# Optimization experiments

Measured on AMD Instinct MI355X. Metric: run time of the kernel, lower is better.

Reference implementation:

```python
import jax, jax.numpy as jnp
import numpy as np

NFILTS = 6  # module-level global in the original repo


def setup_inputs() -> dict:
    key = jax.random.key(0)
    k = jax.random.split(key, 6)
    N, T, D, E = 128, 256, 10, NFILTS
    merged = jax.random.normal(k[0], (N, T, 14), dtype=jnp.float32)
    y_pred_i = jax.random.normal(k[1], (N, T, E), dtype=jnp.float32)
    y_pred_ij = jax.random.normal(k[2], (N, N, T, E), dtype=jnp.float32)
    # input1 holds flux errors in channels [1+nfilts : -2]; keep them bounded away from 0
    input1 = jax.random.uniform(k[3], (N, T, 1 + E + E + 2), dtype=jnp.float32) + 0.5
    samples = jax.random.normal(k[4], (N, D), dtype=jnp.float32)
    labels = jax.random.randint(k[5], (N,), 0, 10, dtype=jnp.int64)
    return {"merged": merged, "y_pred_i": y_pred_i, "y_pred_ij": y_pred_ij,
            "input1": input1, "samples": samples, "labels": labels}


def reference(merged, y_pred_i, y_pred_ij, input1, samples, labels):
    # err_true: [N, T, E]
    err_true = input1[:, :, 1 + NFILTS:-2]
    # pairwise latent distance: S_ij[i,j] = mean_d (samples[j] - samples[i])^2 -> [N, N]
    d = samples[None, :, :] - samples[:, None, :]
    S_ij = jnp.mean(d * d, axis=-1)
    # second term: mean over (T, E) of (y_pred_ij[i,j] - y_pred_i[j])^2 / err_true[j]^2 / 10
    diffsq = jnp.square(y_pred_ij - y_pred_i[None, :, :, :])          # [N, N, T, E]
    second = jnp.mean(diffsq / jnp.square(err_true)[None], axis=(2, 3)) / 10.0  # [N, N]
    avg_term = 0.5 * (second + second.T)
    L_sim = jnp.mean(jnp.abs(S_ij - avg_term))
    return L_sim
```

## Files before the change

### kernel.cpp

```cpp
#include <hip/hip_runtime.h>
#include <hip/hip_bf16.h>

#define NN 128
#define TT 256
#define EE 6
#define DD 10
#define TE (TT*EE)
#define C1 15

__global__ void prep_w(const float* __restrict__ input1, float* __restrict__ w) {
    int idx = blockIdx.x * 256 + threadIdx.x;
    if (idx < NN * TE) {
        int f = idx % TE;
        int j = idx / TE;
        int t = f / EE, e = f % EE;
        float v = input1[(j * TT + t) * C1 + 1 + EE + e];
        w[idx] = 1.0f / (v * v);
    }
}

__launch_bounds__(128)
__global__ void pair_reduce(const float* __restrict__ yij,
                            const float* __restrict__ yi,
                            const float* __restrict__ w,
                            float* __restrict__ raw) {
    const int j = blockIdx.x;
    const int i = blockIdx.y;
    const int tid = threadIdx.x;

    const float4* a  = (const float4*)(yij + ((size_t)i * NN + j) * TE);
    const float4* m  = (const float4*)(yi  + (size_t)j * TE);
    const float4* wv = (const float4*)(w   + (size_t)j * TE);

    float s = 0.0f;
#pragma unroll
    for (int k = 0; k < 3; ++k) {
        int f = tid + k * 128;
        float4 x  = a[f];
        float4 mm = m[f];
        float4 ww = wv[f];
        float d0 = x.x - mm.x; s += d0 * d0 * ww.x;
        float d1 = x.y - mm.y; s += d1 * d1 * ww.y;
        float d2 = x.z - mm.z; s += d2 * d2 * ww.z;
        float d3 = x.w - mm.w; s += d3 * d3 * ww.w;
    }
#pragma unroll
    for (int off = 32; off > 0; off >>= 1) s += __shfl_down(s, off);

    __shared__ float ls[2];
    if ((tid & 63) == 0) ls[tid >> 6] = s;
    __syncthreads();
    if (tid == 0) raw[i * NN + j] = ls[0] + ls[1];
}

__launch_bounds__(256)
__global__ void finalize(const float* __restrict__ raw,
                         const float* __restrict__ samples,
                         float* __restrict__ out) {
    __shared__ float smp[NN * DD];
    for (int k = threadIdx.x; k < NN * DD; k += 256) smp[k] = samples[k];
    __syncthreads();

    const int p = blockIdx.x * 256 + threadIdx.x;
    const int i = p / NN, j = p % NN;

    float S = 0.0f;
#pragma unroll
    for (int d = 0; d < DD; ++d) {
        float dd = smp[j * DD + d] - smp[i * DD + d];
        S += dd * dd;
    }
    S *= (1.0f / DD);

    const float sec = (raw[i * NN + j] + raw[j * NN + i]) * (0.5f / (TE * 10.0f));
    float v = fabsf(S - sec);

#pragma unroll
    for (int off = 32; off > 0; off >>= 1) v += __shfl_down(v, off);

    __shared__ float ls[4];
    const int tid = threadIdx.x;
    if ((tid & 63) == 0) ls[tid >> 6] = v;
    __syncthreads();
    if (tid == 0)
        atomicAdd(out, (ls[0] + ls[1] + ls[2] + ls[3]) * (1.0f / (NN * NN)));
}

extern "C" void kernel_launch(void* const* d_in, const int* in_sizes, int n_in,
                              void* d_out, int out_size, void* d_ws, size_t ws_size,
                              hipStream_t stream) {
    const float* y_pred_i  = (const float*)d_in[1];
    const float* y_pred_ij = (const float*)d_in[2];
    const float* input1    = (const float*)d_in[3];
    const float* samples   = (const float*)d_in[4];
    float* out = (float*)d_out;

    float* w   = (float*)d_ws;
    float* raw = w + (size_t)NN * TE;

    prep_w<<<(NN * TE + 255) / 256, 256, 0, stream>>>(input1, w);

    dim3 grid(NN, NN);
    pair_reduce<<<grid, 128, 0, stream>>>(y_pred_ij, y_pred_i, w, raw);

    hipMemsetAsync(out, 0, sizeof(float), stream);
    finalize<<<64, 256, 0, stream>>>(raw, samples, out);
}
```

Baseline: 162.8 us.

## Map one wavefront per pair tile and finalize in a single block

The pair reduction now gives each 64-lane wavefront a whole (i,j) row of TE elements, with four wavefronts per 256-thread block. This removes the shared-memory and __syncthreads combine and uses four independent accumulators. Finalize runs as one 1024-thread block that writes the output directly, which drops the memset and the atomicAdd, and it stores samples transposed in shared memory. The main kernel reads about 100MB of y_pred_ij, so it is bandwidth bound and the gain is likely small. The single-block finalize also serializes a small tail.

Result: slower. 167.9 us (+3.1%).

```diff
diff --git a/kernel.cpp b/kernel.cpp
--- a/kernel.cpp
+++ b/kernel.cpp
@@ -1,5 +1,4 @@
 #include <hip/hip_runtime.h>
-#include <hip/hip_bf16.h>
 
 #define NN 128
 #define TT 256
@@ -8,7 +7,8 @@
 #define TE (TT*EE)
 #define C1 15
 
-__global__ void prep_w(const float* __restrict__ input1, float* __restrict__ w) {
+__global__ __launch_bounds__(256) void prep_w(const float* __restrict__ input1,
+                                              float* __restrict__ w) {
     int idx = blockIdx.x * 256 + threadIdx.x;
     if (idx < NN * TE) {
         int f = idx % TE;
@@ -19,71 +19,72 @@
     }
 }
 
-__launch_bounds__(128)
-__global__ void pair_reduce(const float* __restrict__ yij,
-                            const float* __restrict__ yi,
-                            const float* __restrict__ w,
-                            float* __restrict__ raw) {
-    const int j = blockIdx.x;
-    const int i = blockIdx.y;
-    const int tid = threadIdx.x;
+__global__ __launch_bounds__(256) void pair_reduce(const float* __restrict__ yij,
+                                                   const float* __restrict__ yi,
+                                                   const float* __restrict__ w,
+                                                   float* __restrict__ raw) {
+    const int lane = threadIdx.x & 63;
+    const int tile = blockIdx.x * 4 + (threadIdx.x >> 6);
+    const int j    = tile & (NN - 1);
 
-    const float4* a  = (const float4*)(yij + ((size_t)i * NN + j) * TE);
-    const float4* m  = (const float4*)(yi  + (size_t)j * TE);
-    const float4* wv = (const float4*)(w   + (size_t)j * TE);
+    const float4* __restrict__ a  = (const float4*)(yij + (size_t)tile * TE);
+    const float4* __restrict__ m  = (const float4*)(yi  + (size_t)j * TE);
+    const float4* __restrict__ wv = (const float4*)(w   + (size_t)j * TE);
 
-    float s = 0.0f;
+    float s0 = 0.0f, s1 = 0.0f, s2 = 0.0f, s3 = 0.0f;
 #pragma unroll
-    for (int k = 0; k < 3; ++k) {
-        int f = tid + k * 128;
+    for (int k = 0; k < 6; ++k) {
+        const int f = lane + k * 64;
         float4 x  = a[f];
         float4 mm = m[f];
         float4 ww = wv[f];
-        float d0 = x.x - mm.x; s += d0 * d0 * ww.x;
-        float d1 = x.y - mm.y; s += d1 * d1 * ww.y;
-        float d2 = x.z - mm.z; s += d2 * d2 * ww.z;
-        float d3 = x.w - mm.w; s += d3 * d3 * ww.w;
+        float d0 = x.x - mm.x; s0 += d0 * d0 * ww.x;
+        float d1 = x.y - mm.y; s1 += d1 * d1 * ww.y;
+        float d2 = x.z - mm.z; s2 += d2 * d2 * ww.z;
+        float d3 = x.w - mm.w; s3 += d3 * d3 * ww.w;
     }
+    float s = (s0 + s1) + (s2 + s3);
 #pragma unroll
     for (int off = 32; off > 0; off >>= 1) s += __shfl_down(s, off);
-
-    __shared__ float ls[2];
-    if ((tid & 63) == 0) ls[tid >> 6] = s;
-    __syncthreads();
-    if (tid == 0) raw[i * NN + j] = ls[0] + ls[1];
+    if (lane == 0) raw[tile] = s;
 }
 
-__launch_bounds__(256)
-__global__ void finalize(const float* __restrict__ raw,
-                         const float* __restrict__ samples,
-                         float* __restrict__ out) {
-    __shared__ float smp[NN * DD];
-    for (int k = threadIdx.x; k < NN * DD; k += 256) smp[k] = samples[k];
+__global__ __launch_bounds__(1024) void finalize(const float* __restrict__ raw,
+                                                 const float* __restrict__ samples,
+                                                 float* __restrict__ out) {
+    __shared__ float smp[DD * NN];
+    for (int k = threadIdx.x; k < NN * DD; k += 1024) {
+        int n = k / DD, d = k % DD;
+        smp[d * NN + n] = samples[k];
+    }
     __syncthreads();
 
-    const int p = blockIdx.x * 256 + threadIdx.x;
-    const int i = p / NN, j = p % NN;
-
-    float S = 0.0f;
+    float v = 0.0f;
 #pragma unroll
-    for (int d = 0; d < DD; ++d) {
-        float dd = smp[j * DD + d] - smp[i * DD + d];
-        S += dd * dd;
+    for (int it = 0; it < (NN * NN) / 1024; ++it) {
+        const int p = it * 1024 + threadIdx.x;
+        const int i = p >> 7, j = p & (NN - 1);
+        float S = 0.0f;
+#pragma unroll
+        for (int d = 0; d < DD; ++d) {
+            float dd = smp[d * NN + j] - smp[d * NN + i];
+            S += dd * dd;
+        }
+        const float sec = (raw[p] + raw[(j << 7) | i]) * (0.5f / (TE * 10.0f));
+        v += fabsf(S * (1.0f / DD) - sec);
     }
-    S *= (1.0f / DD);
-
-    const float sec = (raw[i * NN + j] + raw[j * NN + i]) * (0.5f / (TE * 10.0f));
-    float v = fabsf(S - sec);
 
 #pragma unroll
     for (int off = 32; off > 0; off >>= 1) v += __shfl_down(v, off);
-
-    __shared__ float ls[4];
-    const int tid = threadIdx.x;
-    if ((tid & 63) == 0) ls[tid >> 6] = v;
+    __shared__ float ls[16];
+    if ((threadIdx.x & 63) == 0) ls[threadIdx.x >> 6] = v;
     __syncthreads();
-    if (tid == 0)
-        atomicAdd(out, (ls[0] + ls[1] + ls[2] + ls[3]) * (1.0f / (NN * NN)));
+    if (threadIdx.x == 0) {
+        float t = 0.0f;
+#pragma unroll
+        for (int q = 0; q < 16; ++q) t += ls[q];
+        *out = t * (1.0f / (NN * NN));
+    }
 }
 
 extern "C" void kernel_launch(void* const* d_in, const int* in_sizes, int n_in,
@@ -99,10 +100,6 @@
     float* raw = w + (size_t)NN * TE;
 
     prep_w<<<(NN * TE + 255) / 256, 256, 0, stream>>>(input1, w);
-
-    dim3 grid(NN, NN);
-    pair_reduce<<<grid, 128, 0, stream>>>(y_pred_ij, y_pred_i, w, raw);
-
-    hipMemsetAsync(out, 0, sizeof(float), stream);
-    finalize<<<64, 256, 0, stream>>>(raw, samples, out);
+    pair_reduce<<<(NN * NN) / 4, 256, 0, stream>>>(y_pred_ij, y_pred_i, w, raw);
+    finalize<<<1, 1024, 0, stream>>>(raw, samples, out);
 }
```
